# Kernel tuning notes

Measured on AMD Instinct MI355X. Metric: run time of the kernel, lower is better.

## Reference

```python
import jax, jax.numpy as jnp
import numpy as np
from jax.scipy.special import logsumexp

SINKHORN_ITERS = 3
EPS = 1e-12


def setup_inputs() -> dict:
    key = jax.random.key(0)
    ks = jax.random.split(key, 10)
    B, C, H, W = 32, 384, 48, 48
    HID, D, K = 512, 128, 64
    s = 0.05
    return {
        "x": jax.random.normal(ks[0], (B, C, H, W), dtype=jnp.float32),
        # cluster_features branch: 1x1 convs == per-pixel matmuls
        "w1": jax.random.normal(ks[1], (HID, C), dtype=jnp.float32) * s,
        "b1": jax.random.normal(ks[2], (HID,), dtype=jnp.float32) * s,
        "w2": jax.random.normal(ks[3], (D, HID), dtype=jnp.float32) * s,
        "b2": jax.random.normal(ks[4], (D,), dtype=jnp.float32) * s,
        # score branch
        "s1": jax.random.normal(ks[5], (HID, C), dtype=jnp.float32) * s,
        "c1": jax.random.normal(ks[6], (HID,), dtype=jnp.float32) * s,
        "s2": jax.random.normal(ks[7], (K, HID), dtype=jnp.float32) * s,
        "c2": jax.random.normal(ks[8], (K,), dtype=jnp.float32) * s,
        "alpha": jnp.asarray(1.0, dtype=jnp.float32),  # dust_bin
    }


def _log_optimal_transport(scores, alpha, iters):
    # scores: [b, m, n] with m = num_clusters, n = num tokens
    b, m, n = scores.shape
    norm = -jnp.log(jnp.asarray(m + n, dtype=scores.dtype))
    bins = jnp.broadcast_to(alpha, (b, 1, n)).astype(scores.dtype)
    Z = jnp.concatenate([scores, bins], axis=1)  # [b, m+1, n]
    log_mu = jnp.concatenate([
        jnp.full((m,), norm, dtype=scores.dtype),
        jnp.log(jnp.asarray(n - m, dtype=scores.dtype))[None] + norm,
    ])  # [m+1]
    log_nu = jnp.full((n,), norm, dtype=scores.dtype)
    log_mu = jnp.broadcast_to(log_mu, (b, m + 1))
    log_nu = jnp.broadcast_to(log_nu, (b, n))

    u = jnp.zeros_like(log_mu)
    v = jnp.zeros_like(log_nu)
    for _ in range(iters):
        u = log_mu - logsumexp(Z + v[:, None, :], axis=2)
        v = log_nu - logsumexp(Z + u[:, :, None], axis=1)
    return Z + u[:, :, None] + v[:, None, :] - norm


def reference(x, w1, b1, w2, b2, s1, c1, s2, c2, alpha):
    B, C, H, W = x.shape
    xf = x.reshape(B, C, H * W)  # [b, c, n]
    # cluster features: 1x1 conv -> relu -> 1x1 conv (dropout is identity in eval)
    h = jnp.maximum(jnp.einsum('oc,bcn->bon', w1, xf) + b1[:, None], 0.0)
    f = jnp.einsum('oc,bcn->bon', w2, h) + b2[:, None]  # [b, D, n]
    # scores
    hs = jnp.maximum(jnp.einsum('oc,bcn->bon', s1, xf) + c1[:, None], 0.0)
    p = jnp.einsum('oc,bcn->bon', s2, hs) + c2[:, None]  # [b, K, n]
    # log-domain optimal transport with dust bin
    Z = _log_optimal_transport(p, alpha, SINKHORN_ITERS)
    P = jnp.exp(Z)[:, :-1, :]  # [b, K, n], drop dust bin row
    # repeat-mul-sum pooling == batched contraction over tokens
    agg = jnp.einsum('bdn,bkn->bdk', f, P)  # [b, D, K]
    nrm = jnp.sqrt(jnp.sum(agg * agg, axis=1, keepdims=True))
    agg = agg / jnp.maximum(nrm, EPS)  # L2 normalize over cluster_dim
    return agg.reshape(B, -1)  # [b, D*K]
```

## Files before the change

kernel.cpp:

```cpp
#include <hip/hip_runtime.h>
#include <math.h>
#include <stdint.h>

#define HW_N 2304
#define CB   384
#define HIDD 512
#define HID2 1024
#define DD   128
#define KK   64
#define BATCH 32
#define M1   65
#define NTOK (BATCH * HW_N)
#define NORM_ARG 2368.0f

typedef __bf16 bf16;
typedef __bf16 bf16x8 __attribute__((ext_vector_type(8)));
typedef float  f32x4  __attribute__((ext_vector_type(4)));

__device__ __forceinline__ void gld16(void* lds, const void* g) {
    __builtin_amdgcn_global_load_lds(
        (const __attribute__((address_space(1))) uint32_t*)g,
        (__attribute__((address_space(3))) uint32_t*)lds, 16, 0, 0);
}

template<int N> __device__ __forceinline__ void waitvm() {
    if constexpr (N == 0) asm volatile("s_waitcnt vmcnt(0)" ::: "memory");
    else if constexpr (N == 1) asm volatile("s_waitcnt vmcnt(1)" ::: "memory");
    else if constexpr (N == 2) asm volatile("s_waitcnt vmcnt(2)" ::: "memory");
    else if constexpr (N == 3) asm volatile("s_waitcnt vmcnt(3)" ::: "memory");
    else if constexpr (N == 4) asm volatile("s_waitcnt vmcnt(4)" ::: "memory");
    else if constexpr (N == 5) asm volatile("s_waitcnt vmcnt(5)" ::: "memory");
    else if constexpr (N == 6) asm volatile("s_waitcnt vmcnt(6)" ::: "memory");
    else asm volatile("s_waitcnt vmcnt(0)" ::: "memory");
}

__global__ __launch_bounds__(256)
void x_to_bf16T(const float* __restrict__ x, bf16* __restrict__ xT)
{
    const int b  = blockIdx.z;
    const int n0 = blockIdx.x * 64;
    const int c0 = blockIdx.y * 64;
    __shared__ float t[64][65];
    const int tx = threadIdx.x & 15, ty = threadIdx.x >> 4;
    const float* xb = x + (long)b * CB * HW_N;
    #pragma unroll
    for (int r = 0; r < 64; r += 16) {
        const float4 vv = *(const float4*)&xb[(long)(c0 + r + ty) * HW_N + n0 + tx * 4];
        t[r + ty][tx * 4 + 0] = vv.x; t[r + ty][tx * 4 + 1] = vv.y;
        t[r + ty][tx * 4 + 2] = vv.z; t[r + ty][tx * 4 + 3] = vv.w;
    }
    __syncthreads();
    bf16* ob = xT + (long)b * HW_N * CB;
    #pragma unroll
    for (int r = 0; r < 64; r += 16) {
        const int n = r + ty;
        union { bf16 h[4]; uint2 u2; } pk;
        pk.h[0] = (bf16)t[tx * 4 + 0][n]; pk.h[1] = (bf16)t[tx * 4 + 1][n];
        pk.h[2] = (bf16)t[tx * 4 + 2][n]; pk.h[3] = (bf16)t[tx * 4 + 3][n];
        *(uint2*)&ob[(long)(n0 + n) * CB + c0 + tx * 4] = pk.u2;
    }
}

__device__ __forceinline__ void cvtq(const float* __restrict__ in,
                                     bf16* __restrict__ out, int q)
{
    float4 vv = ((const float4*)in)[q];
    union { bf16 h[4]; uint2 u2; } pk;
    pk.h[0] = (bf16)vv.x; pk.h[1] = (bf16)vv.y;
    pk.h[2] = (bf16)vv.z; pk.h[3] = (bf16)vv.w;
    ((uint2*)out)[q] = pk.u2;
}

__global__ __launch_bounds__(256)
void prep_weights(const float* __restrict__ w1, const float* __restrict__ s1,
                  const float* __restrict__ w2, const float* __restrict__ s2,
                  const float* __restrict__ b1, const float* __restrict__ c1,
                  bf16* __restrict__ Wc, bf16* __restrict__ Wf,
                  float* __restrict__ bc)
{
    const int QW1 = HIDD * CB / 4;
    const int QW2 = DD * HIDD / 4;
    const int QS2 = KK * HIDD / 4;
    int i = blockIdx.x * 256 + threadIdx.x;
    if (i < QW1)                       { cvtq(w1, Wc, i); return; }
    i -= QW1;
    if (i < QW1)                       { cvtq(s1, Wc + (long)HIDD * CB, i); return; }
    i -= QW1;
    if (i < QW2)                       { cvtq(w2, Wf, i); return; }
    i -= QW2;
    if (i < QS2)                       { cvtq(s2, Wf + (long)DD * HIDD, i); return; }
    i -= QS2;
    if (i < 256) {
        float4 vv = (i < 128) ? ((const float4*)b1)[i] : ((const float4*)c1)[i - 128];
        ((float4*)bc)[i] = vv;
    }
}

template<int FA, int FB, int OUT_MODE, bool RELU, int MINW>
__global__ __launch_bounds__(256, MINW)
void mfma_gemm4(const bf16* __restrict__ A, int lda,
                const bf16* __restrict__ B, int ldb,
                const float* __restrict__ bias,
                void* __restrict__ OUT, int ldo,
                int K, int nA)
{
    constexpr int BA = 2 * FA * 16;
    constexpr int BB = 2 * FB * 16;
    constexpr int ROWB = 64;
    constexpr int GA = (BA * ROWB) / 4096;
    constexpr int GB = (BB * ROWB) / 4096;
    constexpr int GAB = GA + GB;

    __shared__ __align__(16) bf16 As[2][BA * 32];
    __shared__ __align__(16) bf16 Bs[2][BB * 32];

    int L = blockIdx.x;
    { const int cpx = gridDim.x >> 3; L = (L & 7) * cpx + (L >> 3); }
    const int ta = L % nA;
    const int tb = L / nA;

    const int tid  = threadIdx.x;
    const int lane = tid & 63;
    const int w    = tid >> 6;
    const int wr   = w >> 1, wc = w & 1;

    const char* Ap = (const char*)A + (long)ta * BA * lda * 2;
    const char* Bp = (const char*)B + (long)tb * BB * ldb * 2;
    const long ldab = (long)lda * 2, ldbb = (long)ldb * 2;

    const int subrow = lane >> 2;
    const int colb   = (lane & 3) << 4;
    const int rl = lane & 15, q = lane >> 4;

    f32x4 acc[FA][FB];
    #pragma unroll
    for (int i = 0; i < FA; i++)
        #pragma unroll
        for (int j = 0; j < FB; j++)
            acc[i][j] = (f32x4){0.f, 0.f, 0.f, 0.f};

    const int nsteps = K / 32;

    auto stageA = [&](int buf, int kt) {
        #pragma unroll
        for (int g = 0; g < GA; ++g) {
            const int ii = g * 4 + w;
            gld16((char*)As[buf] + ii * 1024,
                  Ap + (long)(ii * 16 + subrow) * ldab + (long)kt * ROWB + colb);
        }
    };
    auto stageB = [&](int buf, int kt) {
        #pragma unroll
        for (int g = 0; g < GB; ++g) {
            const int ii = g * 4 + w;
            gld16((char*)Bs[buf] + ii * 1024,
                  Bp + (long)(ii * 16 + subrow) * ldbb + (long)kt * ROWB + colb);
        }
    };

    stageA(0, 0); stageB(0, 0);
    stageA(1, 1); stageB(1, 1);
    waitvm<GAB>();
    __builtin_amdgcn_s_barrier();

    for (int t = 0; t < nsteps; ++t) {
        const int cur = t & 1;
        const char* Ab = (const char*)As[cur];
        const char* Bb = (const char*)Bs[cur];

        bf16x8 a[FA], bb[FB];
        #pragma unroll
        for (int i = 0; i < FA; i++)
            a[i] = *(const bf16x8*)(Ab + (wr * FA * 16 + i * 16 + rl) * ROWB + (q << 4));
        #pragma unroll
        for (int j = 0; j < FB; j++)
            bb[j] = *(const bf16x8*)(Bb + (wc * FB * 16 + j * 16 + rl) * ROWB + (q << 4));

        __builtin_amdgcn_s_setprio(1);
        #pragma unroll
        for (int i = 0; i < FA; i++)
            #pragma unroll
            for (int j = 0; j < FB; j++)
                acc[i][j] = __builtin_amdgcn_mfma_f32_16x16x32_bf16(a[i], bb[j], acc[i][j], 0, 0, 0);
        __builtin_amdgcn_s_setprio(0);

        asm volatile("s_waitcnt lgkmcnt(0)" ::: "memory");
        __builtin_amdgcn_s_barrier();
        if (t + 2 < nsteps) { stageA(cur, t + 2); stageB(cur, t + 2); }
        if (t + 1 < nsteps) {
            if (t + 2 < nsteps) waitvm<GAB>(); else waitvm<0>();
            __builtin_amdgcn_s_barrier();
        }
    }

    const int fr = lane & 15;
    const int fq = lane >> 4;

    if (OUT_MODE == 0) {
        #pragma unroll
        for (int i = 0; i < FA; i++) {
            const int ra0 = ta * BA + wr * FA * 16 + i * 16 + fq * 4;
            const float4 bv = *(const float4*)&bias[ra0];
            #pragma unroll
            for (int j = 0; j < FB; j++) {
                const int rb = tb * BB + wc * FB * 16 + j * 16 + fr;
                union { bf16 h[4]; uint2 u2; } pk;
                float v0 = acc[i][j][0] + bv.x, v1 = acc[i][j][1] + bv.y;
                float v2 = acc[i][j][2] + bv.z, v3 = acc[i][j][3] + bv.w;
                if (RELU) {
                    v0 = fmaxf(v0, 0.f); v1 = fmaxf(v1, 0.f);
                    v2 = fmaxf(v2, 0.f); v3 = fmaxf(v3, 0.f);
                }
                pk.h[0] = (bf16)v0; pk.h[1] = (bf16)v1;
                pk.h[2] = (bf16)v2; pk.h[3] = (bf16)v3;
                *(uint2*)&((bf16*)OUT)[(long)rb * ldo + ra0] = pk.u2;
            }
        }
    } else {
        #pragma unroll
        for (int i = 0; i < FA; i++) {
            const int g0 = ta * BA + wr * FA * 16 + i * 16 + fq * 4;
            const int bi = g0 / HW_N;
            const int nn = g0 - bi * HW_N;
            #pragma unroll
            for (int j = 0; j < FB; j++) {
                const int mg = tb * BB + wc * FB * 16 + j * 16 + fr;
                const float bvs = bias[mg];
                float v0 = acc[i][j][0] + bvs, v1 = acc[i][j][1] + bvs;
                float v2 = acc[i][j][2] + bvs, v3 = acc[i][j][3] + bvs;
                if (RELU) {
                    v0 = fmaxf(v0, 0.f); v1 = fmaxf(v1, 0.f);
                    v2 = fmaxf(v2, 0.f); v3 = fmaxf(v3, 0.f);
                }
                const long base = ((long)bi * ldo + mg) * HW_N + nn;
                if (OUT_MODE == 1) {
                    union { bf16 h[4]; uint2 u2; } pk;
                    pk.h[0] = (bf16)v0; pk.h[1] = (bf16)v1;
                    pk.h[2] = (bf16)v2; pk.h[3] = (bf16)v3;
                    *(uint2*)&((bf16*)OUT)[base] = pk.u2;
                } else {
                    *(float4*)&((float*)OUT)[base] = make_float4(v0, v1, v2, v3);
                }
            }
        }
    }
}

template<bool FIRST>
__global__ __launch_bounds__(256)
void sink_u(const float* __restrict__ Z, const float* __restrict__ v,
            const float* __restrict__ alpha, float* __restrict__ u)
{
    const int b = blockIdx.y;
    const int i = blockIdx.x * 4 + (threadIdx.x >> 6);
    if (i > KK) return;
    const int lane = threadIdx.x & 63;
    const float* zr = Z + ((long)b * KK + i) * HW_N;
    const float* vb = v + (long)b * HW_N;
    const float a = alpha[0];
    float m = -INFINITY, s = 0.f;
    for (int j = lane; j < HW_N; j += 64) {
        float val = (i < KK) ? zr[j] : a;
        if (!FIRST) val += vb[j];
        float mn = fmaxf(m, val);
        s = s * __expf(m - mn) + __expf(val - mn);
        m = mn;
    }
    #pragma unroll
    for (int off = 32; off; off >>= 1) {
        float m2 = __shfl_xor(m, off), s2 = __shfl_xor(s, off);
        float mn = fmaxf(m, m2);
        s = s * __expf(m - mn) + s2 * __expf(m2 - mn);
        m = mn;
    }
    if (lane == 0) {
        const float norm = -logf(NORM_ARG);
        const float logmu = (i < KK) ? norm : (logf((float)(HW_N - KK)) + norm);
        u[b * M1 + i] = logmu - (m + __logf(s));
    }
}

__global__ __launch_bounds__(64)
void sink_v(const float* __restrict__ Z, const float* __restrict__ u,
            const float* __restrict__ alpha, float* __restrict__ v)
{
    const int b = blockIdx.y;
    const int n = blockIdx.x * 64 + threadIdx.x;
    const float* ub = u + b * M1;
    const float* Zb = Z + (long)b * KK * HW_N;
    float m = alpha[0] + ub[KK];
    float s = 1.f;
    for (int i = 0; i < KK; i++) {
        float t = Zb[(long)i * HW_N + n] + ub[i];
        float mn = fmaxf(m, t);
        s = s * __expf(m - mn) + __expf(t - mn);
        m = mn;
    }
    const float norm = -logf(NORM_ARG);
    v[(long)b * HW_N + n] = norm - (m + __logf(s));
}

__global__ __launch_bounds__(256)
void agg_partial(const bf16* __restrict__ f, const float* __restrict__ Z,
                 const float* __restrict__ u, const float* __restrict__ v,
                 float* __restrict__ part)
{
    const int c = blockIdx.x;
    const int b = blockIdx.y;
    const int n0 = c << 8;
    const float norm = -logf(NORM_ARG);

    __shared__ float Fs[16][132];
    __shared__ float Ps[16][68];

    const bf16*  fb = f + (long)b * DD * HW_N;
    const float* Zb = Z + (long)b * KK * HW_N;
    const float* ub = u + b * M1;
    const float* vb = v + (long)b * HW_N;

    const int tid = threadIdx.x;
    const int td = tid & 31;
    const int tk = tid >> 5;

    const int fd = tid >> 1, fh = tid & 1;
    const int pk_ = tid >> 2, pq = tid & 3;

    float acc[4][8] = {};

    for (int nt = 0; nt < 256; nt += 16) {
        {
            union { uint4 u4; unsigned short s[8]; } pv;
            pv.u4 = *(const uint4*)&fb[(long)fd * HW_N + n0 + nt + fh * 8];
            #pragma unroll
            for (int r = 0; r < 8; r++) {
                union { uint32_t q; float fv; } cv;
                cv.q = (uint32_t)pv.s[r] << 16;
                Fs[fh * 8 + r][fd] = cv.fv;
            }
        }
        {
            const int n = n0 + nt + pq * 4;
            const float4 z = *(const float4*)&Zb[(long)pk_ * HW_N + n];
            const float uk = ub[pk_];
            Ps[pq * 4 + 0][pk_] = __expf(z.x + uk + vb[n + 0] - norm);
            Ps[pq * 4 + 1][pk_] = __expf(z.y + uk + vb[n + 1] - norm);
            Ps[pq * 4 + 2][pk_] = __expf(z.z + uk + vb[n + 2] - norm);
            Ps[pq * 4 + 3][pk_] = __expf(z.w + uk + vb[n + 3] - norm);
        }
        __syncthreads();
        #pragma unroll
        for (int nn = 0; nn < 16; nn++) {
            const float4 av = *reinterpret_cast<const float4*>(&Fs[nn][td << 2]);
            const float4 p0 = *reinterpret_cast<const float4*>(&Ps[nn][tk << 3]);
            const float4 p1 = *reinterpret_cast<const float4*>(&Ps[nn][(tk << 3) + 4]);
            float a[4] = {av.x, av.y, av.z, av.w};
            float p[8] = {p0.x, p0.y, p0.z, p0.w, p1.x, p1.y, p1.z, p1.w};
            #pragma unroll
            for (int i = 0; i < 4; i++)
                #pragma unroll
                for (int j = 0; j < 8; j++)
                    acc[i][j] += a[i] * p[j];
        }
        __syncthreads();
    }

    float* pb = part + (long)(b * 9 + c) * (DD * KK);
    #pragma unroll
    for (int i = 0; i < 4; i++) {
        int d = (td << 2) + i;
        float4 o0 = make_float4(acc[i][0], acc[i][1], acc[i][2], acc[i][3]);
        float4 o1 = make_float4(acc[i][4], acc[i][5], acc[i][6], acc[i][7]);
        *reinterpret_cast<float4*>(&pb[d * KK + (tk << 3)]) = o0;
        *reinterpret_cast<float4*>(&pb[d * KK + (tk << 3) + 4]) = o1;
    }
}

__global__ __launch_bounds__(256)
void finalize(const float* __restrict__ part, float* __restrict__ out)
{
    const int b = blockIdx.x;
    __shared__ float agg[DD * KK];
    __shared__ float nrm[KK];
    const int tid = threadIdx.x;

    for (int idx = tid; idx < DD * KK; idx += 256) {
        float s = 0.f;
        #pragma unroll
        for (int cc = 0; cc < 9; cc++)
            s += part[(long)(b * 9 + cc) * (DD * KK) + idx];
        agg[idx] = s;
    }
    __syncthreads();
    if (tid < KK) {
        float ss = 0.f;
        for (int d = 0; d < DD; d++) { float t = agg[d * KK + tid]; ss += t * t; }
        nrm[tid] = fmaxf(sqrtf(ss), 1e-12f);
    }
    __syncthreads();
    for (int idx = tid; idx < DD * KK; idx += 256)
        out[(long)b * (DD * KK) + idx] = agg[idx] / nrm[idx & 63];
}

extern "C" void kernel_launch(void* const* d_in, const int* in_sizes, int n_in,
                              void* d_out, int out_size, void* d_ws, size_t ws_size,
                              hipStream_t stream)
{
    const float* x     = (const float*)d_in[0];
    const float* w1    = (const float*)d_in[1];
    const float* b1    = (const float*)d_in[2];
    const float* w2    = (const float*)d_in[3];
    const float* b2    = (const float*)d_in[4];
    const float* s1    = (const float*)d_in[5];
    const float* c1    = (const float*)d_in[6];
    const float* s2    = (const float*)d_in[7];
    const float* c2    = (const float*)d_in[8];
    const float* alpha = (const float*)d_in[9];
    float* out = (float*)d_out;

    char* p = (char*)d_ws;
    bf16* Wc  = (bf16*)p;  p += (long)HID2 * CB * 2;
    bf16* Wf  = (bf16*)p;  p += (long)(DD + KK) * HIDD * 2;
    float* bc = (float*)p; p += (long)HID2 * 4;
    bf16* xT  = (bf16*)p;  p += (long)NTOK * CB * 2;
    bf16* hs  = (bf16*)p;  p += (long)NTOK * HID2 * 2;
    bf16* f   = (bf16*)p;  p += (long)BATCH * DD * HW_N * 2;
    float* Z  = (float*)p; p += (long)BATCH * KK * HW_N * 4;
    float* u  = (float*)p; p += (long)BATCH * M1 * 4;
    float* v  = (float*)p; p += (long)BATCH * HW_N * 4;
    float* part = (float*)p;

    prep_weights<<<481, 256, 0, stream>>>(w1, s1, w2, s2, b1, c1, Wc, Wf, bc);

    x_to_bf16T<<<dim3(36, 6, 32), 256, 0, stream>>>(x, xT);

    mfma_gemm4<4, 4, 0, true, 4><<<4608, 256, 0, stream>>>(
        Wc, CB, xT, CB, bc, hs, HID2, CB, HID2 / 128);

    mfma_gemm4<4, 4, 1, false, 4><<<NTOK / 128, 256, 0, stream>>>(
        hs, HID2, Wf, HIDD, b2, f, DD, HIDD, NTOK / 128);

    mfma_gemm4<4, 2, 2, false, 4><<<NTOK / 128, 256, 0, stream>>>(
        hs + HIDD, HID2, Wf + (long)DD * HIDD, HIDD, c2, Z, KK, HIDD, NTOK / 128);

    sink_u<true ><<<dim3(17, 32), 256, 0, stream>>>(Z, v, alpha, u);
    sink_v<<<dim3(36, 32), 64, 0, stream>>>(Z, u, alpha, v);
    sink_u<false><<<dim3(17, 32), 256, 0, stream>>>(Z, v, alpha, u);
    sink_v<<<dim3(36, 32), 64, 0, stream>>>(Z, u, alpha, v);
    sink_u<false><<<dim3(17, 32), 256, 0, stream>>>(Z, v, alpha, u);
    sink_v<<<dim3(36, 32), 64, 0, stream>>>(Z, u, alpha, v);

    agg_partial<<<dim3(9, 32), 256, 0, stream>>>(f, Z, u, v, part);
    finalize<<<32, 256, 0, stream>>>(part, out);
}
```

Before: 293.9 us.

## Fuse Sinkhorn iterations into one cooperative kernel with grid syncs

Replaces the six separate sink_u/sink_v launches with a single cooperative kernel that runs all three Sinkhorn iterations, using grid.sync between the row and column log-sum-exp phases. This removes per-launch overhead and the gaps between kernels. In exchange the work is spread over a fixed grid of 512 blocks with grid-stride loops, the sink_v phase now uses 256-thread blocks, and each iteration pays for two grid-wide barriers.

```diff
diff --git a/kernel.cpp b/kernel.cpp
--- a/kernel.cpp
+++ b/kernel.cpp
@@ -1,6 +1,9 @@
 #include <hip/hip_runtime.h>
+#include <hip/hip_cooperative_groups.h>
 #include <math.h>
 #include <stdint.h>
+
+namespace cg = cooperative_groups;
 
 #define HW_N 2304
 #define CB   384
@@ -246,58 +249,60 @@
     }
 }
 
-template<bool FIRST>
 __global__ __launch_bounds__(256)
-void sink_u(const float* __restrict__ Z, const float* __restrict__ v,
-            const float* __restrict__ alpha, float* __restrict__ u)
-{
-    const int b = blockIdx.y;
-    const int i = blockIdx.x * 4 + (threadIdx.x >> 6);
-    if (i > KK) return;
-    const int lane = threadIdx.x & 63;
-    const float* zr = Z + ((long)b * KK + i) * HW_N;
-    const float* vb = v + (long)b * HW_N;
+void sinkhorn_coop(const float* __restrict__ Z, const float* __restrict__ alpha,
+                   float* __restrict__ u, float* __restrict__ v)
+{
+    cg::grid_group grid = cg::this_grid();
     const float a = alpha[0];
-    float m = -INFINITY, s = 0.f;
-    for (int j = lane; j < HW_N; j += 64) {
-        float val = (i < KK) ? zr[j] : a;
-        if (!FIRST) val += vb[j];
-        float mn = fmaxf(m, val);
-        s = s * __expf(m - mn) + __expf(val - mn);
-        m = mn;
-    }
-    #pragma unroll
-    for (int off = 32; off; off >>= 1) {
-        float m2 = __shfl_xor(m, off), s2 = __shfl_xor(s, off);
-        float mn = fmaxf(m, m2);
-        s = s * __expf(m - mn) + s2 * __expf(m2 - mn);
-        m = mn;
-    }
-    if (lane == 0) {
-        const float norm = -logf(NORM_ARG);
-        const float logmu = (i < KK) ? norm : (logf((float)(HW_N - KK)) + norm);
-        u[b * M1 + i] = logmu - (m + __logf(s));
-    }
-}
-
-__global__ __launch_bounds__(64)
-void sink_v(const float* __restrict__ Z, const float* __restrict__ u,
-            const float* __restrict__ alpha, float* __restrict__ v)
-{
-    const int b = blockIdx.y;
-    const int n = blockIdx.x * 64 + threadIdx.x;
-    const float* ub = u + b * M1;
-    const float* Zb = Z + (long)b * KK * HW_N;
-    float m = alpha[0] + ub[KK];
-    float s = 1.f;
-    for (int i = 0; i < KK; i++) {
-        float t = Zb[(long)i * HW_N + n] + ub[i];
-        float mn = fmaxf(m, t);
-        s = s * __expf(m - mn) + __expf(t - mn);
-        m = mn;
-    }
     const float norm = -logf(NORM_ARG);
-    v[(long)b * HW_N + n] = norm - (m + __logf(s));
+    const float logmu_last = logf((float)(HW_N - KK)) + norm;
+    const int lane  = threadIdx.x & 63;
+    const int gwave = (blockIdx.x * blockDim.x + threadIdx.x) >> 6;
+    const int nwave = (gridDim.x * blockDim.x) >> 6;
+    const int gtid  = blockIdx.x * blockDim.x + threadIdx.x;
+    const int gsz   = gridDim.x * blockDim.x;
+
+    for (int it = 0; it < 3; ++it) {
+        for (int row = gwave; row < BATCH * M1; row += nwave) {
+            const int b = row / M1, i = row - b * M1;
+            const float* zr = Z + ((long)b * KK + i) * HW_N;
+            const float* vb = v + (long)b * HW_N;
+            float m = -INFINITY, s = 0.f;
+            for (int j = lane; j < HW_N; j += 64) {
+                float val = (i < KK) ? zr[j] : a;
+                if (it > 0) val += vb[j];
+                float mn = fmaxf(m, val);
+                s = s * __expf(m - mn) + __expf(val - mn);
+                m = mn;
+            }
+            #pragma unroll
+            for (int off = 32; off; off >>= 1) {
+                float m2 = __shfl_xor(m, off), s2 = __shfl_xor(s, off);
+                float mn = fmaxf(m, m2);
+                s = s * __expf(m - mn) + s2 * __expf(m2 - mn);
+                m = mn;
+            }
+            if (lane == 0)
+                u[b * M1 + i] = ((i < KK) ? norm : logmu_last) - (m + __logf(s));
+        }
+        grid.sync();
+        for (int g = gtid; g < BATCH * HW_N; g += gsz) {
+            const int b = g / HW_N, n = g - b * HW_N;
+            const float* ub = u + b * M1;
+            const float* Zb = Z + (long)b * KK * HW_N;
+            float m = a + ub[KK];
+            float s = 1.f;
+            for (int i = 0; i < KK; i++) {
+                float t = Zb[(long)i * HW_N + n] + ub[i];
+                float mn = fmaxf(m, t);
+                s = s * __expf(m - mn) + __expf(t - mn);
+                m = mn;
+            }
+            v[(long)b * HW_N + n] = norm - (m + __logf(s));
+        }
+        grid.sync();
+    }
 }
 
 __global__ __launch_bounds__(256)
@@ -442,12 +447,13 @@
     mfma_gemm4<4, 2, 2, false, 4><<<NTOK / 128, 256, 0, stream>>>(
         hs + HIDD, HID2, Wf + (long)DD * HIDD, HIDD, c2, Z, KK, HIDD, NTOK / 128);
 
-    sink_u<true ><<<dim3(17, 32), 256, 0, stream>>>(Z, v, alpha, u);
-    sink_v<<<dim3(36, 32), 64, 0, stream>>>(Z, u, alpha, v);
-    sink_u<false><<<dim3(17, 32), 256, 0, stream>>>(Z, v, alpha, u);
-    sink_v<<<dim3(36, 32), 64, 0, stream>>>(Z, u, alpha, v);
-    sink_u<false><<<dim3(17, 32), 256, 0, stream>>>(Z, v, alpha, u);
-    sink_v<<<dim3(36, 32), 64, 0, stream>>>(Z, u, alpha, v);
+    {
+        const float* Zp = Z; const float* ap = alpha;
+        float* up = u; float* vp = v;
+        void* args[] = { (void*)&Zp, (void*)&ap, (void*)&up, (void*)&vp };
+        hipLaunchCooperativeKernel((const void*)sinkhorn_coop,
+                                   dim3(512), dim3(256), args, 0, stream);
+    }
 
     agg_partial<<<dim3(9, 32), 256, 0, stream>>>(f, Z, u, v, part);
     finalize<<<32, 256, 0, stream>>>(part, out);
```

Result: slower. 644.2 us (+119.2%).
